# Optimization experiments

Hardware: AMD Instinct MI355X
Metric: run time of the kernel (lower is better)

## Reference

```python
import jax, jax.numpy as jnp
import numpy as np


def setup_inputs() -> dict:
    key = jax.random.key(0)
    k1, k2, k3, k4 = jax.random.split(key, 4)
    B, S, E = 8, 4096, 1024
    H, D = 256, 4  # num_heads, n_wires_per_head; H*D == E
    scale = 1.0 / np.sqrt(E)
    return {
        "x": jax.random.normal(k1, (B, S, E), dtype=jnp.float32),
        "W_proj": jax.random.normal(k2, (E, E), dtype=jnp.float32) * scale,
        "W_combine": jax.random.normal(k3, (E, E), dtype=jnp.float32) * scale,
        "phi": jax.random.normal(k4, (H, D), dtype=jnp.float32),
    }


def reference(x, W_proj, W_combine, phi):
    # Linear projection (no bias): torch Linear computes x @ W.T
    proj = jnp.einsum("bse,fe->bsf", x, W_proj)  # [B,S,E]
    B, S, E = proj.shape
    H, D = phi.shape
    # Quantum head per token: RX-encode each feature, trainable RX, PauliZ measure.
    # RX(a)RX(b) = RX(a+b); <0|RX(t)^dag Z RX(t)|0> = cos(t)  =>  cos(x + phi)
    qout = jnp.cos(proj.reshape(B, S, H, D) + phi)  # broadcast phi[h,d]
    qout = qout.reshape(B, S, E)
    return jnp.einsum("bse,fe->bsf", qout, W_combine)
```

## Files before the change

### kernel.cpp

```cpp
#include <hip/hip_runtime.h>
#include <cstdint>
#include <cstddef>


typedef __attribute__((ext_vector_type(8))) short short8;
typedef __attribute__((ext_vector_type(4))) float f32x4;

__device__ __forceinline__ unsigned short f2bf(float f) {
  unsigned u = __float_as_uint(f);
  u += 0x7FFFu + ((u >> 16) & 1u);
  return (unsigned short)(u >> 16);
}

__device__ __forceinline__ void async_load16(const void* g, const void* l) {
  __builtin_amdgcn_global_load_lds(
      (const __attribute__((address_space(1))) void*)g,
      (__attribute__((address_space(3))) void*)l,
      16, 0, 0);
}

__global__ __launch_bounds__(256) void cast_all(
    const float* __restrict__ x, const float* __restrict__ Wp,
    const float* __restrict__ Wc, unsigned short* __restrict__ xb,
    unsigned short* __restrict__ wpb, unsigned short* __restrict__ wcb) {
  const long nvec = 35651584 / 8;
  for (long v = (long)blockIdx.x * 256 + threadIdx.x; v < nvec;
       v += (long)gridDim.x * 256) {
    const long i = v * 8;
    const float* s;
    unsigned short* d;
    long j;
    if (i < 33554432)      { s = x;  d = xb;  j = i; }
    else if (i < 34603008) { s = Wp; d = wpb; j = i - 33554432; }
    else                   { s = Wc; d = wcb; j = i - 34603008; }
    const float4 a = *(const float4*)(s + j);
    const float4 b = *(const float4*)(s + j + 4);
    ushort4 o0, o1;
    o0.x = f2bf(a.x); o0.y = f2bf(a.y); o0.z = f2bf(a.z); o0.w = f2bf(a.w);
    o1.x = f2bf(b.x); o1.y = f2bf(b.y); o1.z = f2bf(b.z); o1.w = f2bf(b.w);
    *(ushort4*)(d + j) = o0;
    *(ushort4*)(d + j + 4) = o1;
  }
}

constexpr int BM = 256, BN = 256, BK = 64;
constexpr int Kdim = 1024, Ndim = 1024;
constexpr int KT = Kdim / BK;

template <int EPI>
__global__ __launch_bounds__(512, 2) void gemm256(
    const unsigned short* __restrict__ A,
    const unsigned short* __restrict__ B,
    const float* __restrict__ phi,
    void* __restrict__ Cout) {
  __shared__ unsigned short As[2][2][256][32];
  __shared__ unsigned short Bs[2][2][256][32];

  const int tid    = threadIdx.x;
  const int lane   = tid & 63;
  const int wv     = tid >> 6;
  const int wr     = wv >> 2;
  const int wc     = wv & 3;
  const int lane15 = lane & 15;
  const int quad   = lane >> 4;
  const int swz8   = (quad ^ ((lane15 >> 1) & 3)) * 8;

  const int wg   = ((blockIdx.x & 7) << 6) | (blockIdx.x >> 3);
  const long row0 = (long)(wg >> 2) * BM;
  const int  col0 = (wg & 3) * BN;

  const int csrc8 = ((lane & 3) ^ ((lane >> 3) & 3)) * 8;
  const int rA    = wv * 32 + (lane >> 2);

#define SA(KT2, NB, KH)                                                        \
  {                                                                            \
    const unsigned short* g_ =                                                 \
        A + (row0 + rA) * Kdim + (KT2) * BK + (KH) * 32 + csrc8;               \
    async_load16(g_, &As[NB][KH][wv * 32][0]);                                 \
    async_load16(g_ + 16 * Kdim, &As[NB][KH][wv * 32 + 16][0]);                \
  }
#define SB(KT2, NB, KH)                                                        \
  {                                                                            \
    const unsigned short* g_ =                                                 \
        B + (long)(col0 + rA) * Kdim + (KT2) * BK + (KH) * 32 + csrc8;         \
    async_load16(g_, &Bs[NB][KH][wv * 32][0]);                                 \
    async_load16(g_ + 16 * Kdim, &Bs[NB][KH][wv * 32 + 16][0]);                \
  }

  f32x4 acc[8][4];
#pragma unroll
  for (int i = 0; i < 8; ++i)
#pragma unroll
    for (int n = 0; n < 4; ++n) {
      f32x4 z = {0.f, 0.f, 0.f, 0.f};
      acc[i][n] = z;
    }

  SA(0, 0, 0); SB(0, 0, 0);
  SA(0, 0, 1);
  SB(0, 0, 1);
  SA(1, 1, 0);
  SB(1, 1, 0);
  asm volatile("s_waitcnt vmcnt(8)" ::: "memory");
  __builtin_amdgcn_s_barrier();

#pragma unroll 2
  for (int kt = 0; kt < KT; ++kt) {
    const int cur = kt & 1;
    const int nxt = cur ^ 1;
    short8 af[4], bfr[4];

#pragma unroll
    for (int i = 0; i < 4; ++i)
      af[i] = *(const short8*)(&As[cur][0][wr * 128 + i * 16 + lane15][swz8]);
#pragma unroll
    for (int i = 0; i < 4; ++i)
      bfr[i] = *(const short8*)(&Bs[cur][0][wc * 64 + i * 16 + lane15][swz8]);
    if (kt + 1 < KT) SA(kt + 1, nxt, 1)
    __builtin_amdgcn_s_barrier();
    asm volatile("s_waitcnt lgkmcnt(0)" ::: "memory");
    __builtin_amdgcn_sched_barrier(0);
    __builtin_amdgcn_s_setprio(1);
#pragma unroll
    for (int i = 0; i < 4; ++i)
#pragma unroll
      for (int n = 0; n < 4; ++n)
        acc[i][n] = __builtin_amdgcn_mfma_f32_16x16x32_bf16(
            af[i], bfr[n], acc[i][n], 0, 0, 0);
    __builtin_amdgcn_s_setprio(0);
    __builtin_amdgcn_sched_barrier(0);
    __builtin_amdgcn_s_barrier();

#pragma unroll
    for (int i = 0; i < 4; ++i)
      af[i] =
          *(const short8*)(&As[cur][0][wr * 128 + (4 + i) * 16 + lane15][swz8]);
    if (kt + 1 < KT) SB(kt + 1, nxt, 1)
    __builtin_amdgcn_s_barrier();
    asm volatile("s_waitcnt lgkmcnt(0)" ::: "memory");
    __builtin_amdgcn_sched_barrier(0);
    __builtin_amdgcn_s_setprio(1);
#pragma unroll
    for (int i = 0; i < 4; ++i)
#pragma unroll
      for (int n = 0; n < 4; ++n)
        acc[4 + i][n] = __builtin_amdgcn_mfma_f32_16x16x32_bf16(
            af[i], bfr[n], acc[4 + i][n], 0, 0, 0);
    __builtin_amdgcn_s_setprio(0);
    __builtin_amdgcn_sched_barrier(0);
    if (kt < KT - 1) {
      asm volatile("s_waitcnt vmcnt(8)" ::: "memory");
    } else {
      asm volatile("s_waitcnt vmcnt(0)" ::: "memory");
    }
    __builtin_amdgcn_s_barrier();

#pragma unroll
    for (int i = 0; i < 4; ++i)
      af[i] = *(const short8*)(&As[cur][1][wr * 128 + i * 16 + lane15][swz8]);
#pragma unroll
    for (int i = 0; i < 4; ++i)
      bfr[i] = *(const short8*)(&Bs[cur][1][wc * 64 + i * 16 + lane15][swz8]);
    if (kt + 2 < KT) SA(kt + 2, cur, 0)
    __builtin_amdgcn_s_barrier();
    asm volatile("s_waitcnt lgkmcnt(0)" ::: "memory");
    __builtin_amdgcn_sched_barrier(0);
    __builtin_amdgcn_s_setprio(1);
#pragma unroll
    for (int i = 0; i < 4; ++i)
#pragma unroll
      for (int n = 0; n < 4; ++n)
        acc[i][n] = __builtin_amdgcn_mfma_f32_16x16x32_bf16(
            af[i], bfr[n], acc[i][n], 0, 0, 0);
    __builtin_amdgcn_s_setprio(0);
    __builtin_amdgcn_sched_barrier(0);
    __builtin_amdgcn_s_barrier();

#pragma unroll
    for (int i = 0; i < 4; ++i)
      af[i] =
          *(const short8*)(&As[cur][1][wr * 128 + (4 + i) * 16 + lane15][swz8]);
    if (kt + 2 < KT) SB(kt + 2, cur, 0)
    __builtin_amdgcn_s_barrier();
    asm volatile("s_waitcnt lgkmcnt(0)" ::: "memory");
    __builtin_amdgcn_sched_barrier(0);
    __builtin_amdgcn_s_setprio(1);
#pragma unroll
    for (int i = 0; i < 4; ++i)
#pragma unroll
      for (int n = 0; n < 4; ++n)
        acc[4 + i][n] = __builtin_amdgcn_mfma_f32_16x16x32_bf16(
            af[i], bfr[n], acc[4 + i][n], 0, 0, 0);
    __builtin_amdgcn_s_setprio(0);
    __builtin_amdgcn_sched_barrier(0);
    if (kt < KT - 2) {
      asm volatile("s_waitcnt vmcnt(8)" ::: "memory");
    } else if (kt == KT - 2) {
      asm volatile("s_waitcnt vmcnt(4)" ::: "memory");
    }
    __builtin_amdgcn_s_barrier();
  }
#undef SA
#undef SB

  if (EPI == 1) {
    unsigned short* Q = (unsigned short*)Cout;
    float ph[4];
#pragma unroll
    for (int n = 0; n < 4; ++n)
      ph[n] = phi[col0 + wc * 64 + n * 16 + lane15];
#pragma unroll
    for (int mi = 0; mi < 8; ++mi) {
      const long rbase = row0 + wr * 128 + mi * 16 + quad * 4;
#pragma unroll
      for (int n = 0; n < 4; ++n) {
        const int c = col0 + wc * 64 + n * 16 + lane15;
#pragma unroll
        for (int r = 0; r < 4; ++r) {
          float v = __cosf(acc[mi][n][r] + ph[n]);
          Q[(rbase + r) * Ndim + c] = f2bf(v);
        }
      }
    }
  } else {
    float* C = (float*)Cout;
#pragma unroll
    for (int mi = 0; mi < 8; ++mi) {
      const long rbase = row0 + wr * 128 + mi * 16 + quad * 4;
#pragma unroll
      for (int n = 0; n < 4; ++n) {
        const int c = col0 + wc * 64 + n * 16 + lane15;
#pragma unroll
        for (int r = 0; r < 4; ++r)
          C[(rbase + r) * Ndim + c] = acc[mi][n][r];
      }
    }
  }
}

extern "C" void kernel_launch(void* const* d_in, const int* in_sizes, int n_in,
                              void* d_out, int out_size, void* d_ws, size_t ws_size,
                              hipStream_t stream) {
  const float* x   = (const float*)d_in[0];
  const float* Wp  = (const float*)d_in[1];
  const float* Wc  = (const float*)d_in[2];
  const float* phi = (const float*)d_in[3];
  float* out = (float*)d_out;

  char* ws = (char*)d_ws;
  unsigned short* Abf  = (unsigned short*)(ws);
  unsigned short* Qbf  = (unsigned short*)(ws + (size_t)67108864);
  unsigned short* Wpbf = (unsigned short*)(ws + (size_t)134217728);
  unsigned short* Wcbf = (unsigned short*)(ws + (size_t)136314880);

  cast_all<<<4096, 256, 0, stream>>>(x, Wp, Wc, Abf, Wpbf, Wcbf);
  gemm256<1><<<512, 512, 0, stream>>>(Abf, Wpbf, phi, (void*)Qbf);
  gemm256<0><<<512, 512, 0, stream>>>(Qbf, Wcbf, nullptr, (void*)out);

  (void)in_sizes; (void)n_in; (void)out_size; (void)ws_size;
}
```

Measured before the change: 383.8 us.

## Merge GEMM half-steps to cut barriers and widen cast stores

Each K half-tile is now processed as one phase: all 8 A fragments and 4 B fragments are loaded, both A and B async prefetches are issued together, and 32 MFMAs run back to back. This removes several s_barrier and lgkmcnt waits per iteration. The cost is 4 more fragment registers, which may pressure the two-waves-per-SIMD occupancy target, and less interleaving of LDS reads with MFMA. The cast kernel also packs eight bf16 values into a single 16-byte store instead of two 8-byte stores.

```diff
diff --git a/kernel.cpp b/kernel.cpp
--- a/kernel.cpp
+++ b/kernel.cpp
@@ -35,11 +35,12 @@
     else                   { s = Wc; d = wcb; j = i - 34603008; }
     const float4 a = *(const float4*)(s + j);
     const float4 b = *(const float4*)(s + j + 4);
-    ushort4 o0, o1;
-    o0.x = f2bf(a.x); o0.y = f2bf(a.y); o0.z = f2bf(a.z); o0.w = f2bf(a.w);
-    o1.x = f2bf(b.x); o1.y = f2bf(b.y); o1.z = f2bf(b.z); o1.w = f2bf(b.w);
-    *(ushort4*)(d + j) = o0;
-    *(ushort4*)(d + j + 4) = o1;
+    uint4 o;
+    o.x = (unsigned)f2bf(a.x) | ((unsigned)f2bf(a.y) << 16);
+    o.y = (unsigned)f2bf(a.z) | ((unsigned)f2bf(a.w) << 16);
+    o.z = (unsigned)f2bf(b.x) | ((unsigned)f2bf(b.y) << 16);
+    o.w = (unsigned)f2bf(b.z) | ((unsigned)f2bf(b.w) << 16);
+    *(uint4*)(d + j) = o;
   }
 }
 
@@ -97,10 +98,8 @@
     }
 
   SA(0, 0, 0); SB(0, 0, 0);
-  SA(0, 0, 1);
-  SB(0, 0, 1);
-  SA(1, 1, 0);
-  SB(1, 1, 0);
+  SA(0, 0, 1); SB(0, 0, 1);
+  SA(1, 1, 0); SB(1, 1, 0);
   asm volatile("s_waitcnt vmcnt(8)" ::: "memory");
   __builtin_amdgcn_s_barrier();
 
@@ -108,45 +107,24 @@
   for (int kt = 0; kt < KT; ++kt) {
     const int cur = kt & 1;
     const int nxt = cur ^ 1;
-    short8 af[4], bfr[4];
-
-#pragma unroll
-    for (int i = 0; i < 4; ++i)
+    short8 af[8], bfr[4];
+
+#pragma unroll
+    for (int i = 0; i < 8; ++i)
       af[i] = *(const short8*)(&As[cur][0][wr * 128 + i * 16 + lane15][swz8]);
 #pragma unroll
-    for (int i = 0; i < 4; ++i)
-      bfr[i] = *(const short8*)(&Bs[cur][0][wc * 64 + i * 16 + lane15][swz8]);
-    if (kt + 1 < KT) SA(kt + 1, nxt, 1)
-    __builtin_amdgcn_s_barrier();
-    asm volatile("s_waitcnt lgkmcnt(0)" ::: "memory");
-    __builtin_amdgcn_sched_barrier(0);
+    for (int n = 0; n < 4; ++n)
+      bfr[n] = *(const short8*)(&Bs[cur][0][wc * 64 + n * 16 + lane15][swz8]);
+    if (kt + 1 < KT) { SA(kt + 1, nxt, 1) SB(kt + 1, nxt, 1) }
     __builtin_amdgcn_s_setprio(1);
 #pragma unroll
-    for (int i = 0; i < 4; ++i)
+    for (int i = 0; i < 8; ++i)
 #pragma unroll
       for (int n = 0; n < 4; ++n)
         acc[i][n] = __builtin_amdgcn_mfma_f32_16x16x32_bf16(
             af[i], bfr[n], acc[i][n], 0, 0, 0);
     __builtin_amdgcn_s_setprio(0);
-    __builtin_amdgcn_sched_barrier(0);
-    __builtin_amdgcn_s_barrier();
-
-#pragma unroll
-    for (int i = 0; i < 4; ++i)
-      af[i] =
-          *(const short8*)(&As[cur][0][wr * 128 + (4 + i) * 16 + lane15][swz8]);
-    if (kt + 1 < KT) SB(kt + 1, nxt, 1)
-    __builtin_amdgcn_s_barrier();
     asm volatile("s_waitcnt lgkmcnt(0)" ::: "memory");
-    __builtin_amdgcn_sched_barrier(0);
-    __builtin_amdgcn_s_setprio(1);
-#pragma unroll
-    for (int i = 0; i < 4; ++i)
-#pragma unroll
-      for (int n = 0; n < 4; ++n)
-        acc[4 + i][n] = __builtin_amdgcn_mfma_f32_16x16x32_bf16(
-            af[i], bfr[n], acc[4 + i][n], 0, 0, 0);
-    __builtin_amdgcn_s_setprio(0);
     __builtin_amdgcn_sched_barrier(0);
     if (kt < KT - 1) {
       asm volatile("s_waitcnt vmcnt(8)" ::: "memory");
@@ -156,42 +134,21 @@
     __builtin_amdgcn_s_barrier();
 
 #pragma unroll
-    for (int i = 0; i < 4; ++i)
+    for (int i = 0; i < 8; ++i)
       af[i] = *(const short8*)(&As[cur][1][wr * 128 + i * 16 + lane15][swz8]);
 #pragma unroll
-    for (int i = 0; i < 4; ++i)
-      bfr[i] = *(const short8*)(&Bs[cur][1][wc * 64 + i * 16 + lane15][swz8]);
-    if (kt + 2 < KT) SA(kt + 2, cur, 0)
-    __builtin_amdgcn_s_barrier();
-    asm volatile("s_waitcnt lgkmcnt(0)" ::: "memory");
-    __builtin_amdgcn_sched_barrier(0);
+    for (int n = 0; n < 4; ++n)
+      bfr[n] = *(const short8*)(&Bs[cur][1][wc * 64 + n * 16 + lane15][swz8]);
+    if (kt + 2 < KT) { SA(kt + 2, cur, 0) SB(kt + 2, cur, 0) }
     __builtin_amdgcn_s_setprio(1);
 #pragma unroll
-    for (int i = 0; i < 4; ++i)
+    for (int i = 0; i < 8; ++i)
 #pragma unroll
       for (int n = 0; n < 4; ++n)
         acc[i][n] = __builtin_amdgcn_mfma_f32_16x16x32_bf16(
             af[i], bfr[n], acc[i][n], 0, 0, 0);
     __builtin_amdgcn_s_setprio(0);
-    __builtin_amdgcn_sched_barrier(0);
-    __builtin_amdgcn_s_barrier();
-
-#pragma unroll
-    for (int i = 0; i < 4; ++i)
-      af[i] =
-          *(const short8*)(&As[cur][1][wr * 128 + (4 + i) * 16 + lane15][swz8]);
-    if (kt + 2 < KT) SB(kt + 2, cur, 0)
-    __builtin_amdgcn_s_barrier();
     asm volatile("s_waitcnt lgkmcnt(0)" ::: "memory");
-    __builtin_amdgcn_sched_barrier(0);
-    __builtin_amdgcn_s_setprio(1);
-#pragma unroll
-    for (int i = 0; i < 4; ++i)
-#pragma unroll
-      for (int n = 0; n < 4; ++n)
-        acc[4 + i][n] = __builtin_amdgcn_mfma_f32_16x16x32_bf16(
-            af[i], bfr[n], acc[4 + i][n], 0, 0, 0);
-    __builtin_amdgcn_s_setprio(0);
     __builtin_amdgcn_sched_barrier(0);
     if (kt < KT - 2) {
       asm volatile("s_waitcnt vmcnt(8)" ::: "memory");
```

Measured after the change: 371.6 us. 3.2% less time.
